# Optimization experiments

Hardware: AMD Instinct MI355X
Metric: run time of the kernel (lower is better)

The kernel has to match this reference:

```python
import jax, jax.numpy as jnp
import numpy as np

N = 20000          # nodes
E = 320000         # edges (before self loops)
NG = 16            # graphs in batch
DIN = 256          # input_dim = heads*hidden
HID = 64           # hidden_dim
HEADS = 4
EPS = 1e-5         # LayerNorm eps
SLOPE = 0.2        # GATConv leaky_relu negative slope


def _ln(x, g, b):
    mu = jnp.mean(x, -1, keepdims=True)
    var = jnp.mean((x - mu) ** 2, -1, keepdims=True)
    return (x - mu) * jax.lax.rsqrt(var + EPS) * g + b


def _gat(x, src, dst, W, a_src, a_dst, bias, heads, out_dim, concat):
    # x: [N, F]; W: [F, heads*out_dim]; a_src/a_dst: [heads, out_dim]
    h = (x @ W).reshape(-1, heads, out_dim)              # [N, H, D]
    e_s = jnp.sum(h * a_src, -1)                         # [N, H]
    e_d = jnp.sum(h * a_dst, -1)                         # [N, H]
    e = jax.nn.leaky_relu(e_s[src] + e_d[dst], SLOPE)    # [E, H]
    # segment softmax over edges sharing the same target node
    m = jax.ops.segment_max(e, dst, num_segments=N)
    m = jnp.where(jnp.isfinite(m), m, 0.0)
    ex = jnp.exp(e - m[dst])
    s = jax.ops.segment_sum(ex, dst, num_segments=N)
    alpha = ex / (s[dst] + 1e-16)                        # [E, H]
    out = jax.ops.segment_sum(h[src] * alpha[:, :, None], dst, num_segments=N)
    out = out.reshape(-1, heads * out_dim) if concat else out.mean(1)
    return out + bias


def setup_inputs() -> dict:
    key = jax.random.key(0)
    ks = jax.random.split(key, 24)
    sc = 0.05
    inp = {
        "node_x": jax.random.normal(ks[0], (N, DIN), dtype=jnp.float32),
        "edge_index": jax.random.randint(ks[1], (2, E), 0, N, dtype=jnp.int64),
        "batch": jnp.sort(jax.random.randint(ks[2], (N,), 0, NG, dtype=jnp.int64)),
        # layer 1 (concat, heads=4)
        "W1": jax.random.normal(ks[3], (DIN, HEADS * HID), dtype=jnp.float32) * sc,
        "as1": jax.random.normal(ks[4], (HEADS, HID), dtype=jnp.float32) * sc,
        "ad1": jax.random.normal(ks[5], (HEADS, HID), dtype=jnp.float32) * sc,
        "b1": jnp.zeros((HEADS * HID,), dtype=jnp.float32),
        "g1": jnp.ones((HEADS * HID,), dtype=jnp.float32),
        "be1": jnp.zeros((HEADS * HID,), dtype=jnp.float32),
        # layer 2 (concat, heads=4)
        "W2": jax.random.normal(ks[6], (HEADS * HID, HEADS * HID), dtype=jnp.float32) * sc,
        "as2": jax.random.normal(ks[7], (HEADS, HID), dtype=jnp.float32) * sc,
        "ad2": jax.random.normal(ks[8], (HEADS, HID), dtype=jnp.float32) * sc,
        "b2": jnp.zeros((HEADS * HID,), dtype=jnp.float32),
        "g2": jnp.ones((HEADS * HID,), dtype=jnp.float32),
        "be2": jnp.zeros((HEADS * HID,), dtype=jnp.float32),
        # final (heads=1, averaged)
        "Wf": jax.random.normal(ks[9], (HEADS * HID, HID), dtype=jnp.float32) * sc,
        "asf": jax.random.normal(ks[10], (1, HID), dtype=jnp.float32) * sc,
        "adf": jax.random.normal(ks[11], (1, HID), dtype=jnp.float32) * sc,
        "bf": jnp.zeros((HID,), dtype=jnp.float32),
        "gf": jnp.ones((HID,), dtype=jnp.float32),
        "bef": jnp.zeros((HID,), dtype=jnp.float32),
    }
    return inp


def reference(node_x, edge_index, batch, W1, as1, ad1, b1, g1, be1,
              W2, as2, ad2, b2, g2, be2, Wf, asf, adf, bf, gf, bef):
    loops = jnp.arange(N, dtype=edge_index.dtype)
    src = jnp.concatenate([edge_index[0], loops])   # PyG add_self_loops=True
    dst = jnp.concatenate([edge_index[1], loops])

    x = node_x
    # layer 1 + LN + relu + residual (shapes match: DIN == HEADS*HID)
    r = x
    x = _gat(x, src, dst, W1, as1, ad1, b1, HEADS, HID, True)
    x = jax.nn.relu(_ln(x, g1, be1)) + r
    # layer 2
    r = x
    x = _gat(x, src, dst, W2, as2, ad2, b2, HEADS, HID, True)
    x = jax.nn.relu(_ln(x, g2, be2)) + r
    # final layer (heads=1, mean over heads), LN then relu
    x = _gat(x, src, dst, Wf, asf, adf, bf, 1, HID, False)
    x = jax.nn.relu(_ln(x, gf, bef))

    counts = jax.ops.segment_sum(jnp.ones((N,), x.dtype), batch, num_segments=NG)
    mean = jax.ops.segment_sum(x, batch, num_segments=NG) / jnp.clip(counts, 1.0)[:, None]
    mx = jax.ops.segment_max(x, batch, num_segments=NG)
    mx = jnp.where(jnp.isfinite(mx), mx, 0.0)
    pooled = jnp.concatenate([mean, mx], -1)
    return (x, pooled)
```

## Files before the change

### kernel.cpp

```cpp
#include <hip/hip_runtime.h>
#include <cstdint>
#include <cstddef>

#define NN 20000
#define EE 320000
#define TE (EE + NN)
#define NG 16
#define HEADS 4
#define LN_EPS 1e-5f
#define SLOPE 0.2f

typedef __attribute__((ext_vector_type(8))) short bfx8;
typedef __attribute__((ext_vector_type(8))) unsigned short u16x8;
typedef __attribute__((ext_vector_type(4))) float f32x4;
typedef __attribute__((ext_vector_type(8))) float f32x8;

__device__ __forceinline__ short f2bf(float f) {
    unsigned u = __float_as_uint(f);
    u += 0x7FFFu + ((u >> 16) & 1u);
    return (short)(u >> 16);
}
__device__ __forceinline__ float bf2f(unsigned short u) {
    return __uint_as_float(((unsigned)u) << 16);
}
__device__ __forceinline__ float lrelu(float e) {
    return (e >= 0.f) ? e : SLOPE * e;
}

__global__ void deg_kernel(const int* __restrict__ ei, int* __restrict__ counts) {
    int i = blockIdx.x * blockDim.x + threadIdx.x;
    if (i >= TE) return;
    int d = (i < EE) ? ei[EE + i] : (i - EE);
    atomicAdd(&counts[d], 1);
}

__global__ __launch_bounds__(256) void bsum_kernel(const int* __restrict__ cnt,
                                                   int* __restrict__ bsum) {
    int b = blockIdx.x;
    int i = b * 256 + threadIdx.x;
    int v = (i < NN) ? cnt[i] : 0;
    for (int s = 32; s > 0; s >>= 1) v += __shfl_down(v, s);
    __shared__ int ws4[4];
    int lane = threadIdx.x & 63, w = threadIdx.x >> 6;
    if (lane == 0) ws4[w] = v;
    __syncthreads();
    if (threadIdx.x == 0) bsum[b] = ws4[0] + ws4[1] + ws4[2] + ws4[3];
}

__global__ void bscan_kernel(const int* __restrict__ bsum, int* __restrict__ boff, int nb) {
    __shared__ int s[128];
    int t = threadIdx.x;
    int v = (t < nb) ? bsum[t] : 0;
    s[t] = v;
    __syncthreads();
    for (int st = 1; st < 128; st <<= 1) {
        int a = (t >= st) ? s[t - st] : 0;
        __syncthreads();
        s[t] += a;
        __syncthreads();
    }
    if (t < nb) boff[t] = s[t] - v;
}

__global__ __launch_bounds__(256) void offsets_kernel(const int* __restrict__ cnt,
                                                      const int* __restrict__ boff,
                                                      int* __restrict__ off,
                                                      int* __restrict__ cursor) {
    int b = blockIdx.x, t = threadIdx.x;
    int i = b * 256 + t;
    int v = (i < NN) ? cnt[i] : 0;
    int lane = t & 63, w = t >> 6;
    int x = v;
    for (int s = 1; s < 64; s <<= 1) {
        int u = __shfl_up(x, s);
        if (lane >= s) x += u;
    }
    __shared__ int wsum[4];
    if (lane == 63) wsum[w] = x;
    __syncthreads();
    int pre = 0;
    for (int k = 0; k < w; k++) pre += wsum[k];
    int excl = (x + pre - v) + boff[b];
    if (i < NN) { cursor[i] = excl; off[i] = excl; }
    if (i == NN - 1) off[NN] = excl + v;
}

__global__ void csr_fill_kernel(const int* __restrict__ ei, int* __restrict__ cursor,
                                int* __restrict__ csr_src) {
    int i = blockIdx.x * blockDim.x + threadIdx.x;
    if (i >= TE) return;
    int s, d;
    if (i < EE) { s = ei[i]; d = ei[EE + i]; }
    else        { s = i - EE; d = s; }
    int pos = atomicAdd(&cursor[d], 1);
    csr_src[pos] = s;
}

__global__ void gstart_kernel(const int* __restrict__ batch, int* __restrict__ gstart) {
    int g = threadIdx.x;
    if (g > NG) return;
    int lo = 0, hi = NN;
    while (lo < hi) {
        int mid = (lo + hi) >> 1;
        if (batch[mid] < g) lo = mid + 1; else hi = mid;
    }
    gstart[g] = lo;
}

__global__ __launch_bounds__(256) void transpose_all_kernel(
    const float* __restrict__ W1, const float* __restrict__ W2, const float* __restrict__ Wf,
    short* __restrict__ wt1, short* __restrict__ wt2, short* __restrict__ wtf) {
    __shared__ float tile[32][33];
    int z = blockIdx.z;
    const float* W = (z == 0) ? W1 : (z == 1) ? W2 : Wf;
    short* WT = (z == 0) ? wt1 : (z == 1) ? wt2 : wtf;
    int Nc = (z == 2) ? 64 : 256;
    int bx = blockIdx.x * 32;
    int by = blockIdx.y * 32;
    if (bx >= Nc) return;
    int tx = threadIdx.x & 31, ty = threadIdx.x >> 5;
    for (int r = ty; r < 32; r += 8)
        tile[r][tx] = W[(size_t)(by + r) * Nc + bx + tx];
    __syncthreads();
    for (int r = ty; r < 32; r += 8)
        WT[(size_t)(bx + r) * 256 + by + tx] = f2bf(tile[tx][r]);
}

#define GBM 64
#define GBN 64
#define GBK 64
template<bool AF32>
__global__ __launch_bounds__(256) void gemm_attn_kernel(const void* __restrict__ Ap,
                                                        const short* __restrict__ BT,
                                                        unsigned short* __restrict__ Cb,
                                                        float* __restrict__ es,
                                                        float* __restrict__ ed,
                                                        const float* __restrict__ av_src,
                                                        const float* __restrict__ av_dst,
                                                        int M, int K, int Nc, int nheads) {
    __shared__ short Al[GBM * GBK];
    __shared__ short Bl[GBN * GBK];
    __shared__ float sps[64][2];
    __shared__ float spd[64][2];
    const int t = threadIdx.x;
    const int lane = t & 63, wid = t >> 6;
    const int wr = (wid >> 1) * 32, wc = (wid & 1) * 32;
    const int bm = blockIdx.y * GBM, bn = blockIdx.x * GBN;
    const int r0 = t >> 3, ch = t & 7;

    f32x4 acc[2][2] = {};

    for (int k0 = 0; k0 < K; k0 += GBK) {
#pragma unroll
        for (int p = 0; p < 2; p++) {
            int row = p * 32 + r0;
            int arow = bm + row; if (arow >= M) arow = M - 1;
            bfx8 av;
            if constexpr (AF32) {
                const float* A = (const float*)Ap;
                const float* src = A + (size_t)arow * K + k0 + ch * 8;
                float4 f0 = *(const float4*)(src);
                float4 f1 = *(const float4*)(src + 4);
                av[0] = f2bf(f0.x); av[1] = f2bf(f0.y); av[2] = f2bf(f0.z); av[3] = f2bf(f0.w);
                av[4] = f2bf(f1.x); av[5] = f2bf(f1.y); av[6] = f2bf(f1.z); av[7] = f2bf(f1.w);
            } else {
                const short* A = (const short*)Ap;
                av = *(const bfx8*)(A + (size_t)arow * K + k0 + ch * 8);
            }
            bfx8 bv = *(const bfx8*)(BT + (size_t)(bn + row) * K + k0 + ch * 8);
            int wo = (row << 7) + (((ch ^ (row & 7))) << 4);
            *(bfx8*)((char*)Al + wo) = av;
            *(bfx8*)((char*)Bl + wo) = bv;
        }
        __syncthreads();
        bfx8 af[2][2], bfm[2][2];
#pragma unroll
        for (int m = 0; m < 2; m++)
#pragma unroll
            for (int kk = 0; kk < 2; kk++) {
                int rowa = wr + m * 16 + (lane & 15);
                int rowb = wc + m * 16 + (lane & 15);
                int c = kk * 4 + (lane >> 4);
                af[m][kk]  = *(const bfx8*)((const char*)Al + (rowa << 7) + (((c ^ (rowa & 7))) << 4));
                bfm[m][kk] = *(const bfx8*)((const char*)Bl + (rowb << 7) + (((c ^ (rowb & 7))) << 4));
            }
#pragma unroll
        for (int m = 0; m < 2; m++)
#pragma unroll
            for (int n = 0; n < 2; n++) {
                acc[m][n] = __builtin_amdgcn_mfma_f32_16x16x32_bf16(af[m][0], bfm[n][0], acc[m][n], 0, 0, 0);
                acc[m][n] = __builtin_amdgcn_mfma_f32_16x16x32_bf16(af[m][1], bfm[n][1], acc[m][n], 0, 0, 0);
            }
        __syncthreads();
    }

#pragma unroll
    for (int m = 0; m < 2; m++) {
        int row0 = bm + wr + m * 16 + ((lane >> 4) << 2);
#pragma unroll
        for (int n = 0; n < 2; n++) {
            int col = bn + wc + n * 16 + (lane & 15);
#pragma unroll
            for (int j = 0; j < 4; j++) {
                int row = row0 + j;
                if (row < M) Cb[(size_t)row * Nc + col] = (unsigned short)f2bf(acc[m][n][j]);
            }
        }
    }

    const int hd = bn >> 6;
    float asv[2], adv[2];
#pragma unroll
    for (int n = 0; n < 2; n++) {
        int c = wc + n * 16 + (lane & 15);
        asv[n] = av_src[hd * 64 + c];
        adv[n] = av_dst[hd * 64 + c];
    }
#pragma unroll
    for (int m = 0; m < 2; m++) {
#pragma unroll
        for (int j = 0; j < 4; j++) {
            float ps = acc[m][0][j] * asv[0] + acc[m][1][j] * asv[1];
            float pd = acc[m][0][j] * adv[0] + acc[m][1][j] * adv[1];
            ps += __shfl_xor(ps, 1); pd += __shfl_xor(pd, 1);
            ps += __shfl_xor(ps, 2); pd += __shfl_xor(pd, 2);
            ps += __shfl_xor(ps, 4); pd += __shfl_xor(pd, 4);
            ps += __shfl_xor(ps, 8); pd += __shfl_xor(pd, 8);
            if ((lane & 15) == 0) {
                int rl = wr + m * 16 + ((lane >> 4) << 2) + j;
                sps[rl][wid & 1] = ps;
                spd[rl][wid & 1] = pd;
            }
        }
    }
    __syncthreads();
    if (t < 64) {
        int row = bm + t;
        if (row < M) {
            es[(size_t)row * nheads + hd] = sps[t][0] + sps[t][1];
            ed[(size_t)row * nheads + hd] = spd[t][0] + spd[t][1];
        }
    }
}

__global__ __launch_bounds__(256) void gat_agg_ln_kernel(
    const unsigned short* __restrict__ hb,
    const float* __restrict__ es, const float* __restrict__ ed,
    const int* __restrict__ off, const int* __restrict__ csrs,
    const float* __restrict__ bias, const float* __restrict__ gamma, const float* __restrict__ beta,
    const float* __restrict__ residf, const unsigned short* __restrict__ residb,
    unsigned short* __restrict__ xbout) {
    const int wid = threadIdx.x >> 6, lane = threadIdx.x & 63;
    const int n = blockIdx.x * 4 + wid;
    const int half = lane >> 5, sl = lane & 31;
    const int hd = sl >> 3;
    const int d0 = sl * 8;
    const int j0 = off[n], j1 = off[n + 1];
    const float edn = ed[n * HEADS + hd];

    float acc[8] = {};
    float wsum = 0.f;
    int j = j0 + half;
    for (; j + 6 < j1; j += 8) {
        int s0 = csrs[j], s1 = csrs[j + 2], s2 = csrs[j + 4], s3 = csrs[j + 6];
        float w0 = __expf(lrelu(es[s0 * HEADS + hd] + edn));
        float w1 = __expf(lrelu(es[s1 * HEADS + hd] + edn));
        float w2 = __expf(lrelu(es[s2 * HEADS + hd] + edn));
        float w3 = __expf(lrelu(es[s3 * HEADS + hd] + edn));
        u16x8 r0 = *(const u16x8*)(hb + (size_t)s0 * 256 + d0);
        u16x8 r1 = *(const u16x8*)(hb + (size_t)s1 * 256 + d0);
        u16x8 r2 = *(const u16x8*)(hb + (size_t)s2 * 256 + d0);
        u16x8 r3 = *(const u16x8*)(hb + (size_t)s3 * 256 + d0);
        wsum += (w0 + w1) + (w2 + w3);
#pragma unroll
        for (int k = 0; k < 8; k++)
            acc[k] += w0 * bf2f(r0[k]) + w1 * bf2f(r1[k]) + w2 * bf2f(r2[k]) + w3 * bf2f(r3[k]);
    }
    for (; j < j1; j += 2) {
        int s = csrs[j];
        float wt = __expf(lrelu(es[s * HEADS + hd] + edn));
        u16x8 r = *(const u16x8*)(hb + (size_t)s * 256 + d0);
        wsum += wt;
#pragma unroll
        for (int k = 0; k < 8; k++) acc[k] += wt * bf2f(r[k]);
    }
    wsum += __shfl_xor(wsum, 32);
#pragma unroll
    for (int k = 0; k < 8; k++) acc[k] += __shfl_xor(acc[k], 32);

    float inv = 1.f / (wsum + 1e-16f);
    f32x8 bi = *(const f32x8*)(bias + d0);
    float v[8];
    float ls = 0.f, lq = 0.f;
#pragma unroll
    for (int k = 0; k < 8; k++) {
        v[k] = acc[k] * inv + bi[k];
        ls += v[k];
        lq += v[k] * v[k];
    }
    ls += __shfl_xor(ls, 1);  lq += __shfl_xor(lq, 1);
    ls += __shfl_xor(ls, 2);  lq += __shfl_xor(lq, 2);
    ls += __shfl_xor(ls, 4);  lq += __shfl_xor(lq, 4);
    ls += __shfl_xor(ls, 8);  lq += __shfl_xor(lq, 8);
    ls += __shfl_xor(ls, 16); lq += __shfl_xor(lq, 16);
    float mu = ls * (1.0f / 256.0f);
    float var = lq * (1.0f / 256.0f) - mu * mu;
    float rstd = rsqrtf(var + LN_EPS);
    f32x8 ga = *(const f32x8*)(gamma + d0);
    f32x8 be = *(const f32x8*)(beta + d0);
    f32x8 rs = {};
    if (half == 0) {
        if (residf) {
            rs = *(const f32x8*)(residf + (size_t)n * 256 + d0);
        } else {
            u16x8 rb = *(const u16x8*)(residb + (size_t)n * 256 + d0);
#pragma unroll
            for (int k = 0; k < 8; k++) rs[k] = bf2f(rb[k]);
        }
    }
    float y[8];
#pragma unroll
    for (int k = 0; k < 8; k++) {
        float yy = fmaxf((v[k] - mu) * rstd * ga[k] + be[k], 0.f) + rs[k];
        float tt = __shfl_xor(yy, 32);
        y[k] = half ? tt : yy;
    }
    if (half == 1) {
        u16x8 ob;
#pragma unroll
        for (int k = 0; k < 8; k++) ob[k] = (unsigned short)f2bf(y[k]);
        *(u16x8*)(xbout + (size_t)n * 256 + d0) = ob;
    }
}

__global__ __launch_bounds__(256) void gat_final_kernel(
    const unsigned short* __restrict__ hb,
    const float* __restrict__ es, const float* __restrict__ ed,
    const int* __restrict__ off, const int* __restrict__ csrs,
    const float* __restrict__ bias, const float* __restrict__ gamma, const float* __restrict__ beta,
    float* __restrict__ xout) {
    const int wid = threadIdx.x >> 6, lane = threadIdx.x & 63;
    const int n = blockIdx.x * 4 + wid;
    const int q = lane >> 4, sq = lane & 15;
    const int d0 = sq * 4;
    const int j0 = off[n], j1 = off[n + 1];
    const float edn = ed[n];

    float acc[4] = {};
    float wsum = 0.f;
    int j = j0 + q;
    for (; j + 4 < j1; j += 8) {
        int s0 = csrs[j], s1 = csrs[j + 4];
        float w0 = __expf(lrelu(es[s0] + edn));
        float w1 = __expf(lrelu(es[s1] + edn));
        ushort4 r0 = *(const ushort4*)(hb + (size_t)s0 * 64 + d0);
        ushort4 r1 = *(const ushort4*)(hb + (size_t)s1 * 64 + d0);
        wsum += w0 + w1;
        acc[0] += w0 * bf2f(r0.x) + w1 * bf2f(r1.x);
        acc[1] += w0 * bf2f(r0.y) + w1 * bf2f(r1.y);
        acc[2] += w0 * bf2f(r0.z) + w1 * bf2f(r1.z);
        acc[3] += w0 * bf2f(r0.w) + w1 * bf2f(r1.w);
    }
    for (; j < j1; j += 4) {
        int s = csrs[j];
        float wt = __expf(lrelu(es[s] + edn));
        ushort4 r = *(const ushort4*)(hb + (size_t)s * 64 + d0);
        wsum += wt;
        acc[0] += wt * bf2f(r.x);
        acc[1] += wt * bf2f(r.y);
        acc[2] += wt * bf2f(r.z);
        acc[3] += wt * bf2f(r.w);
    }
    wsum += __shfl_xor(wsum, 16);
    wsum += __shfl_xor(wsum, 32);
#pragma unroll
    for (int k = 0; k < 4; k++) {
        acc[k] += __shfl_xor(acc[k], 16);
        acc[k] += __shfl_xor(acc[k], 32);
    }
    float inv = 1.f / (wsum + 1e-16f);
    float4 bi = *(const float4*)(bias + d0);
    float v[4];
    float ls = 0.f, lq = 0.f;
    v[0] = acc[0] * inv + bi.x; v[1] = acc[1] * inv + bi.y;
    v[2] = acc[2] * inv + bi.z; v[3] = acc[3] * inv + bi.w;
#pragma unroll
    for (int k = 0; k < 4; k++) { ls += v[k]; lq += v[k] * v[k]; }
    ls += __shfl_xor(ls, 1); lq += __shfl_xor(lq, 1);
    ls += __shfl_xor(ls, 2); lq += __shfl_xor(lq, 2);
    ls += __shfl_xor(ls, 4); lq += __shfl_xor(lq, 4);
    ls += __shfl_xor(ls, 8); lq += __shfl_xor(lq, 8);
    float mu = ls * (1.0f / 64.0f);
    float var = lq * (1.0f / 64.0f) - mu * mu;
    float rstd = rsqrtf(var + LN_EPS);
    if (q == 0) {
        float4 ga = *(const float4*)(gamma + d0);
        float4 be = *(const float4*)(beta + d0);
        float4 o;
        o.x = fmaxf((v[0] - mu) * rstd * ga.x + be.x, 0.f);
        o.y = fmaxf((v[1] - mu) * rstd * ga.y + be.y, 0.f);
        o.z = fmaxf((v[2] - mu) * rstd * ga.z + be.z, 0.f);
        o.w = fmaxf((v[3] - mu) * rstd * ga.w + be.w, 0.f);
        *(float4*)(xout + (size_t)n * 64 + d0) = o;
    }
}

__global__ __launch_bounds__(256) void pool_partial_kernel(
    const float* __restrict__ x, const int* __restrict__ gstart,
    float* __restrict__ gsum, unsigned* __restrict__ gmax) {
    int g = blockIdx.x, sp = blockIdx.y;
    int r0 = gstart[g], r1 = gstart[g + 1];
    int t = threadIdx.x, d = t & 63, rg = t >> 6;
    float sum = 0.f, mx = 0.f;
    for (int r = r0 + sp * 4 + rg; r < r1; r += 32) {
        float v = x[(size_t)r * 64 + d];
        sum += v;
        mx = fmaxf(mx, v);
    }
    __shared__ float S[256], M[256];
    S[t] = sum; M[t] = mx;
    __syncthreads();
    if (t < 64) {
        float s4 = S[t] + S[t + 64] + S[t + 128] + S[t + 192];
        float m4 = fmaxf(fmaxf(M[t], M[t + 64]), fmaxf(M[t + 128], M[t + 192]));
        atomicAdd(&gsum[g * 64 + t], s4);
        atomicMax(&gmax[g * 64 + t], __float_as_uint(m4));
    }
}

__global__ void pool_final_kernel(const float* __restrict__ gsum,
                                  const unsigned* __restrict__ gmax,
                                  const int* __restrict__ gstart,
                                  float* __restrict__ pout) {
    int g = blockIdx.x, d = threadIdx.x;
    float c = fmaxf((float)(gstart[g + 1] - gstart[g]), 1.0f);
    pout[g * 128 + d] = gsum[g * 64 + d] / c;
    pout[g * 128 + 64 + d] = __uint_as_float(gmax[g * 64 + d]);
}

extern "C" void kernel_launch(void* const* d_in, const int* in_sizes, int n_in,
                              void* d_out, int out_size, void* d_ws, size_t ws_size,
                              hipStream_t stream) {
    const float* node_x = (const float*)d_in[0];
    const int*   ei     = (const int*)d_in[1];
    const int*   batch  = (const int*)d_in[2];
    const float* W1  = (const float*)d_in[3];
    const float* as1 = (const float*)d_in[4];
    const float* ad1 = (const float*)d_in[5];
    const float* b1  = (const float*)d_in[6];
    const float* g1  = (const float*)d_in[7];
    const float* be1 = (const float*)d_in[8];
    const float* W2  = (const float*)d_in[9];
    const float* as2 = (const float*)d_in[10];
    const float* ad2 = (const float*)d_in[11];
    const float* b2  = (const float*)d_in[12];
    const float* g2  = (const float*)d_in[13];
    const float* be2 = (const float*)d_in[14];
    const float* Wf  = (const float*)d_in[15];
    const float* asf = (const float*)d_in[16];
    const float* adf = (const float*)d_in[17];
    const float* bf  = (const float*)d_in[18];
    const float* gf  = (const float*)d_in[19];
    const float* bef = (const float*)d_in[20];
    float* out = (float*)d_out;

    char* w = (char*)d_ws;
    auto alloc = [&](size_t bytes) -> void* {
        void* p = (void*)w;
        w += (bytes + 255) & ~(size_t)255;
        return p;
    };
    unsigned short* hb   = (unsigned short*)alloc((size_t)NN * 256 * 2);
    unsigned short* xbA  = (unsigned short*)alloc((size_t)NN * 256 * 2);
    unsigned short* xbB  = (unsigned short*)alloc((size_t)NN * 256 * 2);
    short*          wt1  = (short*)alloc((size_t)256 * 256 * 2);
    short*          wt2  = (short*)alloc((size_t)256 * 256 * 2);
    short*          wtf  = (short*)alloc((size_t)64 * 256 * 2);
    float*          es   = (float*)alloc((size_t)NN * HEADS * 4);
    float*          ed   = (float*)alloc((size_t)NN * HEADS * 4);
    int*      counts = (int*)alloc((size_t)NN * 4);
    int*      off    = (int*)alloc((size_t)(NN + 1) * 4);
    int*      cursor = (int*)alloc((size_t)NN * 4);
    int*      csrs   = (int*)alloc((size_t)TE * 4);
    int*      bsum   = (int*)alloc((size_t)128 * 4);
    int*      boff   = (int*)alloc((size_t)128 * 4);
    float*    gsum   = (float*)alloc((size_t)NG * 64 * 4);
    unsigned* gmax   = (unsigned*)alloc((size_t)NG * 64 * 4);
    int*      gstart = (int*)alloc((size_t)(NG + 1) * 4);

    hipMemsetAsync(counts, 0, (size_t)NN * 4, stream);
    hipMemsetAsync(gsum, 0, (size_t)NG * 64 * 4, stream);
    hipMemsetAsync(gmax, 0, (size_t)NG * 64 * 4, stream);

    const int NB = (NN + 255) / 256;
    const int EB = (TE + 255) / 256;

    deg_kernel<<<EB, 256, 0, stream>>>(ei, counts);
    bsum_kernel<<<NB, 256, 0, stream>>>(counts, bsum);
    bscan_kernel<<<1, 128, 0, stream>>>(bsum, boff, NB);
    offsets_kernel<<<NB, 256, 0, stream>>>(counts, boff, off, cursor);
    csr_fill_kernel<<<EB, 256, 0, stream>>>(ei, cursor, csrs);
    gstart_kernel<<<1, 32, 0, stream>>>(batch, gstart);

    transpose_all_kernel<<<dim3(8, 8, 3), 256, 0, stream>>>(W1, W2, Wf, wt1, wt2, wtf);

    dim3 gg256(4, (NN + GBM - 1) / GBM);
    dim3 gg64(1, (NN + GBM - 1) / GBM);

    gemm_attn_kernel<true><<<gg256, 256, 0, stream>>>(node_x, wt1, hb, es, ed, as1, ad1, NN, 256, 256, HEADS);
    gat_agg_ln_kernel<<<NN / 4, 256, 0, stream>>>(hb, es, ed, off, csrs, b1, g1, be1, node_x, nullptr, xbB);
    gemm_attn_kernel<false><<<gg256, 256, 0, stream>>>(xbB, wt2, hb, es, ed, as2, ad2, NN, 256, 256, HEADS);
    gat_agg_ln_kernel<<<NN / 4, 256, 0, stream>>>(hb, es, ed, off, csrs, b2, g2, be2, nullptr, xbB, xbA);
    gemm_attn_kernel<false><<<gg64, 256, 0, stream>>>(xbA, wtf, hb, es, ed, asf, adf, NN, 256, 64, 1);
    gat_final_kernel<<<NN / 4, 256, 0, stream>>>(hb, es, ed, off, csrs, bf, gf, bef, out);
    pool_partial_kernel<<<dim3(NG, 8), 256, 0, stream>>>(out, gstart, gsum, gmax);
    pool_final_kernel<<<NG, 64, 0, stream>>>(gsum, gmax, gstart, out + (size_t)NN * 64);
}
```

Measured before the change: 277.4 us.

## Double GEMM row tile to 128 and merge small setup launches

The GEMM+attention kernel now computes 128 rows per block instead of 64. Each wave holds two row halves, so every B fragment loaded from LDS is reused across twice as many MFMAs, and the block count is halved. Separately, the gstart binary search is folded into the block-scan kernel, and the three memsets become one by placing counts, gsum and gmax next to each other in the workspace. The larger tile raises LDS and register use per block and leaves fewer blocks to spread over the GPU.

```diff
diff --git a/kernel.cpp b/kernel.cpp
--- a/kernel.cpp
+++ b/kernel.cpp
@@ -47,9 +47,18 @@
     if (threadIdx.x == 0) bsum[b] = ws4[0] + ws4[1] + ws4[2] + ws4[3];
 }
 
-__global__ void bscan_kernel(const int* __restrict__ bsum, int* __restrict__ boff, int nb) {
+__global__ void bscan_kernel(const int* __restrict__ bsum, int* __restrict__ boff, int nb,
+                             const int* __restrict__ batch, int* __restrict__ gstart) {
     __shared__ int s[128];
     int t = threadIdx.x;
+    if (t <= NG) {
+        int g = t, lo = 0, hi = NN;
+        while (lo < hi) {
+            int mid = (lo + hi) >> 1;
+            if (batch[mid] < g) lo = mid + 1; else hi = mid;
+        }
+        gstart[g] = lo;
+    }
     int v = (t < nb) ? bsum[t] : 0;
     s[t] = v;
     __syncthreads();
@@ -94,17 +103,6 @@
     else        { s = i - EE; d = s; }
     int pos = atomicAdd(&cursor[d], 1);
     csr_src[pos] = s;
-}
-
-__global__ void gstart_kernel(const int* __restrict__ batch, int* __restrict__ gstart) {
-    int g = threadIdx.x;
-    if (g > NG) return;
-    int lo = 0, hi = NN;
-    while (lo < hi) {
-        int mid = (lo + hi) >> 1;
-        if (batch[mid] < g) lo = mid + 1; else hi = mid;
-    }
-    gstart[g] = lo;
 }
 
 __global__ __launch_bounds__(256) void transpose_all_kernel(
@@ -126,7 +124,7 @@
         WT[(size_t)(bx + r) * 256 + by + tx] = f2bf(tile[tx][r]);
 }
 
-#define GBM 64
+#define GBM 128
 #define GBN 64
 #define GBK 64
 template<bool AF32>
@@ -140,19 +138,19 @@
                                                         int M, int K, int Nc, int nheads) {
     __shared__ short Al[GBM * GBK];
     __shared__ short Bl[GBN * GBK];
-    __shared__ float sps[64][2];
-    __shared__ float spd[64][2];
+    __shared__ float sps[128][2];
+    __shared__ float spd[128][2];
     const int t = threadIdx.x;
     const int lane = t & 63, wid = t >> 6;
     const int wr = (wid >> 1) * 32, wc = (wid & 1) * 32;
     const int bm = blockIdx.y * GBM, bn = blockIdx.x * GBN;
     const int r0 = t >> 3, ch = t & 7;
 
-    f32x4 acc[2][2] = {};
+    f32x4 acc[2][2][2] = {};
 
     for (int k0 = 0; k0 < K; k0 += GBK) {
 #pragma unroll
-        for (int p = 0; p < 2; p++) {
+        for (int p = 0; p < 4; p++) {
             int row = p * 32 + r0;
             int arow = bm + row; if (arow >= M) arow = M - 1;
             bfx8 av;
@@ -167,46 +165,63 @@
                 const short* A = (const short*)Ap;
                 av = *(const bfx8*)(A + (size_t)arow * K + k0 + ch * 8);
             }
+            int wo = (row << 7) + (((ch ^ (row & 7))) << 4);
+            *(bfx8*)((char*)Al + wo) = av;
+        }
+#pragma unroll
+        for (int p = 0; p < 2; p++) {
+            int row = p * 32 + r0;
             bfx8 bv = *(const bfx8*)(BT + (size_t)(bn + row) * K + k0 + ch * 8);
             int wo = (row << 7) + (((ch ^ (row & 7))) << 4);
-            *(bfx8*)((char*)Al + wo) = av;
             *(bfx8*)((char*)Bl + wo) = bv;
         }
         __syncthreads();
-        bfx8 af[2][2], bfm[2][2];
-#pragma unroll
-        for (int m = 0; m < 2; m++)
+        bfx8 af[2][2][2], bfm[2][2];
+#pragma unroll
+        for (int n = 0; n < 2; n++)
 #pragma unroll
             for (int kk = 0; kk < 2; kk++) {
-                int rowa = wr + m * 16 + (lane & 15);
-                int rowb = wc + m * 16 + (lane & 15);
+                int rowb = wc + n * 16 + (lane & 15);
                 int c = kk * 4 + (lane >> 4);
-                af[m][kk]  = *(const bfx8*)((const char*)Al + (rowa << 7) + (((c ^ (rowa & 7))) << 4));
-                bfm[m][kk] = *(const bfx8*)((const char*)Bl + (rowb << 7) + (((c ^ (rowb & 7))) << 4));
+                bfm[n][kk] = *(const bfx8*)((const char*)Bl + (rowb << 7) + (((c ^ (rowb & 7))) << 4));
             }
 #pragma unroll
-        for (int m = 0; m < 2; m++)
+        for (int h = 0; h < 2; h++)
+#pragma unroll
+            for (int m = 0; m < 2; m++)
+#pragma unroll
+                for (int kk = 0; kk < 2; kk++) {
+                    int rowa = h * 64 + wr + m * 16 + (lane & 15);
+                    int c = kk * 4 + (lane >> 4);
+                    af[h][m][kk] = *(const bfx8*)((const char*)Al + (rowa << 7) + (((c ^ (rowa & 7))) << 4));
+                }
+#pragma unroll
+        for (int h = 0; h < 2; h++)
+#pragma unroll
+            for (int m = 0; m < 2; m++)
+#pragma unroll
+                for (int n = 0; n < 2; n++) {
+                    acc[h][m][n] = __builtin_amdgcn_mfma_f32_16x16x32_bf16(af[h][m][0], bfm[n][0], acc[h][m][n], 0, 0, 0);
+                    acc[h][m][n] = __builtin_amdgcn_mfma_f32_16x16x32_bf16(af[h][m][1], bfm[n][1], acc[h][m][n], 0, 0, 0);
+                }
+        __syncthreads();
+    }
+
+#pragma unroll
+    for (int h = 0; h < 2; h++)
+#pragma unroll
+        for (int m = 0; m < 2; m++) {
+            int row0 = bm + h * 64 + wr + m * 16 + ((lane >> 4) << 2);
 #pragma unroll
             for (int n = 0; n < 2; n++) {
-                acc[m][n] = __builtin_amdgcn_mfma_f32_16x16x32_bf16(af[m][0], bfm[n][0], acc[m][n], 0, 0, 0);
-                acc[m][n] = __builtin_amdgcn_mfma_f32_16x16x32_bf16(af[m][1], bfm[n][1], acc[m][n], 0, 0, 0);
+                int col = bn + wc + n * 16 + (lane & 15);
+#pragma unroll
+                for (int j = 0; j < 4; j++) {
+                    int row = row0 + j;
+                    if (row < M) Cb[(size_t)row * Nc + col] = (unsigned short)f2bf(acc[h][m][n][j]);
+                }
             }
-        __syncthreads();
-    }
-
-#pragma unroll
-    for (int m = 0; m < 2; m++) {
-        int row0 = bm + wr + m * 16 + ((lane >> 4) << 2);
-#pragma unroll
-        for (int n = 0; n < 2; n++) {
-            int col = bn + wc + n * 16 + (lane & 15);
-#pragma unroll
-            for (int j = 0; j < 4; j++) {
-                int row = row0 + j;
-                if (row < M) Cb[(size_t)row * Nc + col] = (unsigned short)f2bf(acc[m][n][j]);
-            }
-        }
-    }
+        }
 
     const int hd = bn >> 6;
     float asv[2], adv[2];
@@ -217,24 +232,26 @@
         adv[n] = av_dst[hd * 64 + c];
     }
 #pragma unroll
-    for (int m = 0; m < 2; m++) {
-#pragma unroll
-        for (int j = 0; j < 4; j++) {
-            float ps = acc[m][0][j] * asv[0] + acc[m][1][j] * asv[1];
-            float pd = acc[m][0][j] * adv[0] + acc[m][1][j] * adv[1];
-            ps += __shfl_xor(ps, 1); pd += __shfl_xor(pd, 1);
-            ps += __shfl_xor(ps, 2); pd += __shfl_xor(pd, 2);
-            ps += __shfl_xor(ps, 4); pd += __shfl_xor(pd, 4);
-            ps += __shfl_xor(ps, 8); pd += __shfl_xor(pd, 8);
-            if ((lane & 15) == 0) {
-                int rl = wr + m * 16 + ((lane >> 4) << 2) + j;
-                sps[rl][wid & 1] = ps;
-                spd[rl][wid & 1] = pd;
+    for (int h = 0; h < 2; h++)
+#pragma unroll
+        for (int m = 0; m < 2; m++) {
+#pragma unroll
+            for (int j = 0; j < 4; j++) {
+                float ps = acc[h][m][0][j] * asv[0] + acc[h][m][1][j] * asv[1];
+                float pd = acc[h][m][0][j] * adv[0] + acc[h][m][1][j] * adv[1];
+                ps += __shfl_xor(ps, 1); pd += __shfl_xor(pd, 1);
+                ps += __shfl_xor(ps, 2); pd += __shfl_xor(pd, 2);
+                ps += __shfl_xor(ps, 4); pd += __shfl_xor(pd, 4);
+                ps += __shfl_xor(ps, 8); pd += __shfl_xor(pd, 8);
+                if ((lane & 15) == 0) {
+                    int rl = h * 64 + wr + m * 16 + ((lane >> 4) << 2) + j;
+                    sps[rl][wid & 1] = ps;
+                    spd[rl][wid & 1] = pd;
+                }
             }
         }
-    }
     __syncthreads();
-    if (t < 64) {
+    if (t < 128) {
         int row = bm + t;
         if (row < M) {
             es[(size_t)row * nheads + hd] = sps[t][0] + sps[t][1];
@@ -479,28 +496,26 @@
     float*          es   = (float*)alloc((size_t)NN * HEADS * 4);
     float*          ed   = (float*)alloc((size_t)NN * HEADS * 4);
     int*      counts = (int*)alloc((size_t)NN * 4);
+    float*    gsum   = (float*)alloc((size_t)NG * 64 * 4);
+    unsigned* gmax   = (unsigned*)alloc((size_t)NG * 64 * 4);
+    char*     zero_end = w;
     int*      off    = (int*)alloc((size_t)(NN + 1) * 4);
     int*      cursor = (int*)alloc((size_t)NN * 4);
     int*      csrs   = (int*)alloc((size_t)TE * 4);
     int*      bsum   = (int*)alloc((size_t)128 * 4);
     int*      boff   = (int*)alloc((size_t)128 * 4);
-    float*    gsum   = (float*)alloc((size_t)NG * 64 * 4);
-    unsigned* gmax   = (unsigned*)alloc((size_t)NG * 64 * 4);
     int*      gstart = (int*)alloc((size_t)(NG + 1) * 4);
 
-    hipMemsetAsync(counts, 0, (size_t)NN * 4, stream);
-    hipMemsetAsync(gsum, 0, (size_t)NG * 64 * 4, stream);
-    hipMemsetAsync(gmax, 0, (size_t)NG * 64 * 4, stream);
+    hipMemsetAsync(counts, 0, (size_t)(zero_end - (char*)counts), stream);
 
     const int NB = (NN + 255) / 256;
     const int EB = (TE + 255) / 256;
 
     deg_kernel<<<EB, 256, 0, stream>>>(ei, counts);
     bsum_kernel<<<NB, 256, 0, stream>>>(counts, bsum);
-    bscan_kernel<<<1, 128, 0, stream>>>(bsum, boff, NB);
+    bscan_kernel<<<1, 128, 0, stream>>>(bsum, boff, NB, batch, gstart);
     offsets_kernel<<<NB, 256, 0, stream>>>(counts, boff, off, cursor);
     csr_fill_kernel<<<EB, 256, 0, stream>>>(ei, cursor, csrs);
-    gstart_kernel<<<1, 32, 0, stream>>>(batch, gstart);
 
     transpose_all_kernel<<<dim3(8, 8, 3), 256, 0, stream>>>(W1, W2, Wf, wt1, wt2, wtf);
 
```

Result: no change. 281.8 us (+1.6%).
